# Kernel tuning notes

Measured on AMD Instinct MI355X. Metric: run time of the kernel, lower is better.

Reference implementation:

```python
import jax, jax.numpy as jnp
from jax import lax
import numpy as np

# Model hyperparameters (match init_kwargs)
DIM = 128
D_STATE = 16
D_CONV = 4
EXPAND = 2
NSLICES = 4
D_INNER = DIM * EXPAND        # 256
DT_RANK = DIM // 16           # 8
B_SZ, H_IMG, W_IMG = 2, 64, 64


def setup_inputs() -> dict:
    key = jax.random.key(0)
    ks = jax.random.split(key, 32)
    def nrm(i, shape, s=0.02):
        return jax.random.normal(ks[i], shape, jnp.float32) * s
    A_init = jnp.log(jnp.tile(jnp.arange(1, D_STATE + 1, dtype=jnp.float32)[None, :], (D_INNER, 1)))
    inp = {}
    inp["x"] = jax.random.normal(ks[0], (B_SZ, DIM, H_IMG, W_IMG), jnp.float32)
    inp["ln_w"] = jnp.ones((DIM,), jnp.float32)
    inp["ln_b"] = jnp.zeros((DIM,), jnp.float32)
    inp["in_proj_w"] = nrm(1, (2 * D_INNER, DIM))
    i = 2
    for s in ("f", "b", "s"):
        inp[f"conv_w_{s}"] = nrm(i, (D_INNER, 1, D_CONV), 0.1); i += 1
        inp[f"conv_b_{s}"] = jnp.zeros((D_INNER,), jnp.float32)
        inp[f"xproj_w_{s}"] = nrm(i, (DT_RANK + 2 * D_STATE, D_INNER)); i += 1
        inp[f"dtproj_w_{s}"] = nrm(i, (D_INNER, DT_RANK), 0.1); i += 1
        inp[f"dtproj_b_{s}"] = nrm(i, (D_INNER,), 0.1) - 4.0; i += 1  # softplus -> small dt
        inp[f"A_log_{s}"] = A_init
        inp[f"D_{s}"] = jnp.ones((D_INNER,), jnp.float32)
    inp["out_proj_w"] = nrm(i, (DIM, D_INNER)); i += 1
    inp["fuse1_w"] = nrm(i, (DIM, 2 * DIM, 3, 3), 0.05); i += 1
    inp["fuse1_b"] = jnp.zeros((DIM,), jnp.float32)
    inp["fuse2_w"] = nrm(i, (DIM, 2 * DIM, 3, 3), 0.05); i += 1
    inp["fuse2_b"] = jnp.zeros((DIM,), jnp.float32)
    return inp


def causal_conv1d(u, w, b):
    # u: (B, L, d); depthwise causal conv over L, kernel (d, 1, K)
    xc = jnp.swapaxes(u, 1, 2)  # (B, d, L)
    xc = jnp.pad(xc, ((0, 0), (0, 0), (w.shape[-1] - 1, 0)))
    y = lax.conv_general_dilated(xc, w, (1,), 'VALID',
                                 dimension_numbers=('NCH', 'OIH', 'NCH'),
                                 feature_group_count=w.shape[0])
    return jnp.swapaxes(y, 1, 2) + b


def selective_scan(u, delta, A, Bm, Cm, D):
    # u, delta: (B, L, d); A: (d, n); Bm, Cm: (B, L, n)
    dA = jnp.exp(delta[..., None] * A)                       # (B, L, d, n)
    dBu = (delta * u)[..., None] * Bm[:, :, None, :]         # (B, L, d, n)
    dA = jnp.moveaxis(dA, 1, 0)                              # (L, B, d, n)
    dBu = jnp.moveaxis(dBu, 1, 0)
    def step(h, xs):
        a, bu = xs
        h = a * h + bu
        return h, h
    h0 = jnp.zeros(dA.shape[1:], dA.dtype)
    _, hs = lax.scan(step, h0, (dA, dBu))                    # hs: (L, B, d, n)
    y = jnp.einsum('lbdn,bln->bld', hs, Cm)
    return y + u * D


def mamba_branch(u, cw, cb, xw, dw, db, A_log, D):
    # u: (B, L, d_inner)
    uc = jax.nn.silu(causal_conv1d(u, cw, cb))
    proj = uc @ xw.T                                         # (B, L, dt_rank + 2*n)
    dt = proj[..., :DT_RANK]
    Bm = proj[..., DT_RANK:DT_RANK + D_STATE]
    Cm = proj[..., DT_RANK + D_STATE:]
    delta = jax.nn.softplus(dt @ dw.T + db)
    return selective_scan(uc, delta, -jnp.exp(A_log), Bm, Cm, D)


def conv2d_3x3(x, w, b):
    y = lax.conv_general_dilated(x, w, (1, 1), ((1, 1), (1, 1)),
                                 dimension_numbers=('NCHW', 'OIHW', 'NCHW'))
    return y + b[None, :, None, None]


def reference(x, ln_w, ln_b, in_proj_w,
              conv_w_f, conv_b_f, xproj_w_f, dtproj_w_f, dtproj_b_f, A_log_f, D_f,
              conv_w_b, conv_b_b, xproj_w_b, dtproj_w_b, dtproj_b_b, A_log_b, D_b,
              conv_w_s, conv_b_s, xproj_w_s, dtproj_w_s, dtproj_b_s, A_log_s, D_s,
              out_proj_w, fuse1_w, fuse1_b, fuse2_w, fuse2_b):
    Bn, C, H, W = x.shape
    L = H * W
    xf = jnp.swapaxes(x.reshape(Bn, C, L), 1, 2)             # (B, L, C)
    mu = xf.mean(-1, keepdims=True)
    var = xf.var(-1, keepdims=True)
    xn = (xf - mu) / jnp.sqrt(var + 1e-5) * ln_w + ln_b
    xz = xn @ in_proj_w.T                                    # (B, L, 2*d_inner)
    u, z = xz[..., :D_INNER], xz[..., D_INNER:]
    # bimamba v3: forward, backward, and slice-permuted scans
    perm = jnp.arange(L).reshape(NSLICES, L // NSLICES).T.reshape(-1)
    inv = jnp.argsort(perm)
    y_f = mamba_branch(u, conv_w_f, conv_b_f, xproj_w_f, dtproj_w_f, dtproj_b_f, A_log_f, D_f)
    y_b = mamba_branch(u[:, ::-1], conv_w_b, conv_b_b, xproj_w_b, dtproj_w_b, dtproj_b_b, A_log_b, D_b)[:, ::-1]
    y_s = mamba_branch(u[:, perm], conv_w_s, conv_b_s, xproj_w_s, dtproj_w_s, dtproj_b_s, A_log_s, D_s)[:, inv]
    q, k, v = y_f, y_b, y_s                                  # (B, L, d_inner) each
    y = (y_f + y_b + y_s) * jax.nn.silu(z)
    out = y @ out_proj_w.T                                   # (B, L, dim)
    # channel-wise global attention: (q^T k) softmax over channels, then v @ attn^T
    attn = jax.nn.softmax(jnp.einsum('bld,ble->bde', q, k), axis=-1)  # (B, D, D)
    out_a = jnp.einsum('bld,bed->ble', v, attn)              # (B, L, d_inner)
    out_a = out_a.reshape(Bn, -1, H, W)                      # matches torch .view(B,-1,H,W)
    out_a = conv2d_3x3(out_a, fuse1_w, fuse1_b)              # (B, dim, H, W)
    out_m = jnp.swapaxes(out, 1, 2).reshape(Bn, C, H, W)
    o = conv2d_3x3(jnp.concatenate([out_a, out_m], axis=1), fuse2_w, fuse2_b)
    return o + x
```

## Files before the change

### kernel.cpp

```cpp
#include <hip/hip_runtime.h>
#include <math.h>

#define B_SZ 2
#define CDIM 128
#define LSEQ 4096
#define DIN  256
#define NPROJ 40
#define NCH  128
#define CHL  (LSEQ / NCH)
#define KSPL 16
#define DIRPJ 327680

typedef float f32x4 __attribute__((ext_vector_type(4)));
typedef short s16x8 __attribute__((ext_vector_type(8)));

__device__ __forceinline__ float silu_f(float v) { return v / (1.f + __expf(-v)); }

__device__ __forceinline__ unsigned short f2bf(float x) {
  unsigned int u = __float_as_uint(x);
  u += 0x7fff + ((u >> 16) & 1);
  return (unsigned short)(u >> 16);
}
__device__ __forceinline__ float bf2f(unsigned short u) {
  return __uint_as_float(((unsigned int)u) << 16);
// ... 52 lines not shown
    #pragma unroll 8
    for (int j = 0; j < 32; ++j) { float v = sx[part * 32 + j][row]; s += v; s2 += v * v; }
    s += __shfl_xor(s, 1); s += __shfl_xor(s, 2);
    s2 += __shfl_xor(s2, 1); s2 += __shfl_xor(s2, 2);
    float mu = s * (1.f / 128.f);
    float rstd = rsqrtf(s2 * (1.f / 128.f) - mu * mu + 1e-5f);
    unsigned short* o = xnbf + ((size_t)bb * 4096 + t0 + row) * 128 + part * 32;
    #pragma unroll
    for (int j = 0; j < 32; j += 2) {
      int c = part * 32 + j;
      float v0 = (sx[c][row] - mu) * rstd * lnw[c] + lnb[c];
      float v1 = (sx[c + 1][row] - mu) * rstd * lnw[c + 1] + lnb[c + 1];
      unsigned int pk = (unsigned int)f2bf(v0) | ((unsigned int)f2bf(v1) << 16);
      *(unsigned int*)(o + j) = pk;
    }
  } else {
    int zi = (bx - 960) * 256 + tid;
    ((uint4*)padz)[zi] = make_uint4(0, 0, 0, 0);
  }
}

__global__ __launch_bounds__(256) void gemm_mfma_nt(
    const unsigned short* __restrict__ A, const unsigned short* __restrict__ Bm,
    float* __restrict__ C, unsigned short* __restrict__ Cbf, int M, int N, int K,
    long sAb, long sBb, long sCb, int mode, int chofs) {
  A += (long)blockIdx.z * sAb; Bm += (long)blockIdx.z * sBb;
  if (mode == 1) Cbf += (long)blockIdx.z * sCb;
  else if (mode == 0) C += (long)blockIdx.z * sCb;
  int m0 = blockIdx.x * 64, n0 = blockIdx.y * 64;
  int tid = threadIdx.x;
  int wv = tid >> 6, lane = tid & 63, col = lane & 15, g = lane >> 4;
  __shared__ unsigned short As[8192];
  __shared__ unsigned short Bs[8192];
  f32x4 acc[4] = {};
  for (int k0 = 0; k0 < K; k0 += 128) {
    __syncthreads();
    #pragma unroll
    for (int i = 0; i < 4; ++i) {
      int s = tid + i * 256;
      int m = s >> 4, kg = s & 15;
      int off = (m * 256 + kg * 16) ^ ((m & 7) << 4);
      uint4 va = *(const uint4*)(A + (size_t)(m0 + m) * K + k0 + kg * 8);
      *(uint4*)((char*)As + off) = va;
      uint4 vb = *(const uint4*)(Bm + (size_t)(n0 + m) * K + k0 + kg * 8);
      *(uint4*)((char*)Bs + off) = vb;
    }
    __syncthreads();
    #pragma unroll
    for (int ks = 0; ks < 4; ++ks) {
      int arow = wv * 16 + col;
      s16x8 a = *(const s16x8*)((const char*)As +
                 ((arow * 256 + ks * 64 + g * 16) ^ ((col & 7) << 4)));
      #pragma unroll
      for (int nf = 0; nf < 4; ++nf) {
        int brow = nf * 16 + col;
        s16x8 bf = *(const s16x8*)((const char*)Bs +
                   ((brow * 256 + ks * 64 + g * 16) ^ ((col & 7) << 4)));
        acc[nf] = __builtin_amdgcn_mfma_f32_16x16x32_bf16(a, bf, acc[nf], 0, 0, 0);
      }
    }
  }
  #pragma unroll
  for (int nf = 0; nf < 4; ++nf) {
    #pragma unroll
    for (int r = 0; r < 4; ++r) {
      int m = m0 + wv * 16 + g * 4 + r;
      int n = n0 + nf * 16 + col;
      if (n >= N) continue;
      if (mode == 0) C[(size_t)m * N + n] = acc[nf][r];
      else if (mode == 1) Cbf[(size_t)m * N + n] = f2bf(acc[nf][r]);
      else {
        int b2 = blockIdx.z + (m >> 12);
        int sp = m & 4095;
        size_t o = (((size_t)b2 * 66 + (sp >> 6) + 1) * 66 + (sp & 63) + 1) * 256 + chofs + n;
        Cbf[o] = f2bf(acc[nf][r]);
      }
    }
  }
}

__global__ __launch_bounds__(256) void gemm_xc(
    const unsigned short* __restrict__ xzbf,
    const float* __restrict__ cw0, const float* __restrict__ cw1, const float* __restrict__ cw2,
    const float* __restrict__ cb0, const float* __restrict__ cb1, const float* __restrict__ cb2,
    const unsigned short* __restrict__ xwpackbf,
    float* __restrict__ proj, unsigned short* __restrict__ ucbf) {
  int dir = blockIdx.z;
  int m0 = blockIdx.x * 64;
  int tid = threadIdx.x;
  int wv = tid >> 6, lane = tid & 63, col = lane & 15, g = lane >> 4;
  const float* cw = dir == 0 ? cw0 : dir == 1 ? cw1 : cw2;
  const float* cb = dir == 0 ? cb0 : dir == 1 ? cb1 : cb2;
  __shared__ unsigned short As[8192];
  __shared__ unsigned short Bs[8192];
  __shared__ float scw[256 * 5];
  #pragma unroll
  for (int t = 0; t < 4; ++t) scw[tid * 5 + t] = cw[tid * 4 + t];
  scw[tid * 5 + 4] = cb[tid];
  const unsigned short* xwd = xwpackbf + dir * 16384;
// ... 40 lines not shown
      int arow = wv * 16 + col;
      s16x8 a = *(const s16x8*)((const char*)As +
                 ((arow * 256 + ks * 64 + g * 16) ^ ((col & 7) << 4)));
      #pragma unroll
      for (int nf = 0; nf < 4; ++nf) {
        int brow = nf * 16 + col;
        s16x8 bf = *(const s16x8*)((const char*)Bs +
                   ((brow * 256 + ks * 64 + g * 16) ^ ((col & 7) << 4)));
        acc[nf] = __builtin_amdgcn_mfma_f32_16x16x32_bf16(a, bf, acc[nf], 0, 0, 0);
      }
    }
  }
  #pragma unroll
  for (int nf = 0; nf < 4; ++nf) {
    #pragma unroll
    for (int r = 0; r < 4; ++r) {
      int m = m0 + wv * 16 + g * 4 + r;
      int n = nf * 16 + col;
      if (n < NPROJ) proj[(size_t)dir * DIRPJ + (size_t)m * NPROJ + n] = acc[nf][r];
    }
  }
}

__global__ __launch_bounds__(256) void post_scan(
    const unsigned short* __restrict__ ybf, const unsigned short* __restrict__ xzbf,
    const unsigned short* __restrict__ Bm, unsigned short* __restrict__ Cbf,
    unsigned short* __restrict__ yT) {
  __shared__ unsigned short As[8192];
  __shared__ unsigned short Bs[8192];
  __shared__ unsigned short T[64][72];
  int id = blockIdx.x;
  int tid = threadIdx.x;
  if (id >= 256) {
    int t = id - 256;
    int lt = t & 63, rest = t >> 6;
    int dt = rest & 3, p = rest >> 2;
    int l0 = lt * 64, d0 = dt * 64;
    const unsigned short* src = ybf + ((size_t)p * 4096) * 256;
    #pragma unroll
    for (int i = 0; i < 2; ++i) {
      int idx = tid + i * 256;
      int l = idx >> 3, dg = idx & 7;
      uint4 v = *(const uint4*)(src + (size_t)(l0 + l) * 256 + d0 + dg * 8);
      const unsigned short* pv = (const unsigned short*)&v;
      #pragma unroll
      for (int j = 0; j < 8; ++j) T[dg * 8 + j][l] = pv[j];
    }
    __syncthreads();
    #pragma unroll
    for (int i = 0; i < 2; ++i) {
      int idx = tid + i * 256;
      int d = idx >> 3, lg = idx & 7;
      uint4 v = *(const uint4*)&T[d][lg * 8];
      *(uint4*)(yT + ((size_t)p * 256 + d0 + d) * 4096 + l0 + lg * 8) = v;
    }
    return;
  }
  const size_t ds = (size_t)B_SZ * LSEQ * DIN;
  int m0 = (id >> 1) * 64, n0 = (id & 1) * 64;
  int wv = tid >> 6, lane = tid & 63, col = lane & 15, g = lane >> 4;
  f32x4 acc[4] = {};
  for (int k0 = 0; k0 < 256; k0 += 128) {
    __syncthreads();
    #pragma unroll
    for (int i = 0; i < 4; ++i) {
      int s = tid + i * 256;
      int m = s >> 4, kg = s & 15;
      size_t row = m0 + m;
      size_t ai = row * 256 + k0 + kg * 8;
      uint4 va = *(const uint4*)(ybf + ai);
      uint4 vb = *(const uint4*)(ybf + ds + ai);
      uint4 vc = *(const uint4*)(ybf + 2 * ds + ai);
      uint4 vz = *(const uint4*)(xzbf + row * 512 + 256 + k0 + kg * 8);
      const unsigned short* pa = (const unsigned short*)&va;
      const unsigned short* pb = (const unsigned short*)&vb;
      const unsigned short* pc = (const unsigned short*)&vc;
      const unsigned short* pz = (const unsigned short*)&vz;
      unsigned int pk[4];
      #pragma unroll
      for (int j = 0; j < 8; j += 2) {
        float w0 = (bf2f(pa[j]) + bf2f(pb[j]) + bf2f(pc[j])) * silu_f(bf2f(pz[j]));
        float w1 = (bf2f(pa[j+1]) + bf2f(pb[j+1]) + bf2f(pc[j+1])) * silu_f(bf2f(pz[j+1]));
        pk[j >> 1] = (unsigned int)f2bf(w0) | ((unsigned int)f2bf(w1) << 16);
      }
      int off = (m * 256 + kg * 16) ^ ((m & 7) << 4);
      *(uint4*)((char*)As + off) = make_uint4(pk[0], pk[1], pk[2], pk[3]);
      uint4 wb = *(const uint4*)(Bm + (size_t)(n0 + m) * 256 + k0 + kg * 8);
      *(uint4*)((char*)Bs + off) = wb;
    }
    __syncthreads();
    #pragma unroll
    for (int ks = 0; ks < 4; ++ks) {
      int arow = wv * 16 + col;
      s16x8 a = *(const s16x8*)((const char*)As +
                 ((arow * 256 + ks * 64 + g * 16) ^ ((col & 7) << 4)));
      #pragma unroll
      for (int nf = 0; nf < 4; ++nf) {
        int brow = nf * 16 + col;
        s16x8 bf = *(const s16x8*)((const char*)Bs +
                   ((brow * 256 + ks * 64 + g * 16) ^ ((col & 7) << 4)));
        acc[nf] = __builtin_amdgcn_mfma_f32_16x16x32_bf16(a, bf, acc[nf], 0, 0, 0);
      }
    }
  }
  #pragma unroll
  for (int nf = 0; nf < 4; ++nf) {
    #pragma unroll
    for (int r = 0; r < 4; ++r) {
      int m = m0 + wv * 16 + g * 4 + r;
      int n = n0 + nf * 16 + col;
      int b2 = m >> 12;
      int sp = m & 4095;
      size_t o = (((size_t)b2 * 66 + (sp >> 6) + 1) * 66 + (sp & 63) + 1) * 256 + 128 + n;
      Cbf[o] = f2bf(acc[nf][r]);
    }
  }
}

__global__ __launch_bounds__(256) void gemm_ts(
    const unsigned short* __restrict__ yT, float* __restrict__ P) {
  int bz = blockIdx.z;
  int b = bz / KSPL, s = bz % KSPL;
  const unsigned short* A  = yT + (size_t)b * 256 * 4096;
  const unsigned short* Bm = yT + (size_t)(2 + b) * 256 * 4096;
  float* Pb = P + (size_t)bz * 65536;
  int m0 = blockIdx.x * 64, n0 = blockIdx.y * 64;
  int tid = threadIdx.x;
  int wv = tid >> 6, lane = tid & 63, col = lane & 15, g = lane >> 4;
  __shared__ unsigned short As[8192];
  __shared__ unsigned short Bs[8192];
  f32x4 acc[4] = {};
  int kb = s * 256;
  for (int k0 = kb; k0 < kb + 256; k0 += 128) {
    __syncthreads();
    #pragma unroll
    for (int i = 0; i < 4; ++i) {
      int sI = tid + i * 256;
      int m = sI >> 4, kg = sI & 15;
      int off = (m * 256 + kg * 16) ^ ((m & 7) << 4);
      uint4 va = *(const uint4*)(A + (size_t)(m0 + m) * 4096 + k0 + kg * 8);
      *(uint4*)((char*)As + off) = va;
      uint4 vb = *(const uint4*)(Bm + (size_t)(n0 + m) * 4096 + k0 + kg * 8);
      *(uint4*)((char*)Bs + off) = vb;
    }
    __syncthreads();
    #pragma unroll
    for (int ks = 0; ks < 4; ++ks) {
      int arow = wv * 16 + col;
      s16x8 a = *(const s16x8*)((const char*)As +
                 ((arow * 256 + ks * 64 + g * 16) ^ ((col & 7) << 4)));
      #pragma unroll
      for (int nf = 0; nf < 4; ++nf) {
        int brow = nf * 16 + col;
        s16x8 bf = *(const s16x8*)((const char*)Bs +
                   ((brow * 256 + ks * 64 + g * 16) ^ ((col & 7) << 4)));
        acc[nf] = __builtin_amdgcn_mfma_f32_16x16x32_bf16(a, bf, acc[nf], 0, 0, 0);
      }
    }
  }
  #pragma unroll
  for (int nf = 0; nf < 4; ++nf)
    #pragma unroll
    for (int r = 0; r < 4; ++r) {
      int m = m0 + wv * 16 + g * 4 + r;
      int n = n0 + nf * 16 + col;
      Pb[(size_t)m * 256 + n] = acc[nf][r];
    }
}

__global__ __launch_bounds__(256) void attn_reduce_softmax(
    const float* __restrict__ P, unsigned short* __restrict__ attnbf) {
  int row = blockIdx.x;
  int b = row >> 8, d = row & 255;
  int t = threadIdx.x;
  const float* p = P + ((size_t)b * KSPL) * 65536 + (size_t)d * 256 + t;
  float v = 0.f;
  #pragma unroll
  for (int s = 0; s < KSPL; ++s) v += p[(size_t)s * 65536];
  __shared__ float red[256];
  red[t] = v; __syncthreads();
  for (int s = 128; s > 0; s >>= 1) { if (t < s) red[t] = fmaxf(red[t], red[t + s]); __syncthreads(); }
  float mx = red[0]; __syncthreads();
  float e = __expf(v - mx);
  red[t] = e; __syncthreads();
  for (int s = 128; s > 0; s >>= 1) { if (t < s) red[t] += red[t + s]; __syncthreads(); }
  attnbf[(size_t)row * 256 + t] = f2bf(e / red[0]);
}

__global__ __launch_bounds__(256) void scan_part1(
    const unsigned short* __restrict__ uc, const float* __restrict__ proj,
    const float* __restrict__ al0, const float* __restrict__ al1, const float* __restrict__ al2,
    const float* __restrict__ dw0, const float* __restrict__ dw1, const float* __restrict__ dw2,
    const float* __restrict__ db0, const float* __restrict__ db1, const float* __restrict__ db2,
    float* __restrict__ hend, float* __restrict__ sdsum) {
  int chunk = blockIdx.x, b = blockIdx.y, dir = blockIdx.z;
  int d = threadIdx.x;
  const float* alog = dir == 0 ? al0 : dir == 1 ? al1 : al2;
  const float* dwp  = dir == 0 ? dw0 : dir == 1 ? dw1 : dw2;
  const float* dbp  = dir == 0 ? db0 : dir == 1 ? db1 : db2;
  float An0 = -__expf(alog[d * 16]) * 1.44269504f;
  float dwr[8];
  #pragma unroll
  for (int i = 0; i < 8; ++i) dwr[i] = dwp[d * 8 + i];
  float dbv = dbp[d];
  size_t base = (((size_t)dir * B_SZ + b) * LSEQ + (size_t)chunk * CHL);
  const unsigned short* ucp = uc + base * DIN + d;
  const float* prj = proj + base * NPROJ;
  __shared__ float sPr[CHL][NPROJ];
  for (int i = threadIdx.x; i < CHL * NPROJ; i += 256)
    sPr[i / NPROJ][i % NPROJ] = prj[i];
  __syncthreads();
  float h[16];
  #pragma unroll
  for (int n = 0; n < 16; ++n) h[n] = 0.f;
  float sd = 0.f;
  float uv = bf2f(ucp[0]);
  for (int l = 0; l < CHL; ++l) {
    float uvn = (l + 1 < CHL) ? bf2f(ucp[(size_t)(l + 1) * DIN]) : 0.f;
    float a = dbv;
    #pragma unroll
    for (int i = 0; i < 8; ++i) a += sPr[l][i] * dwr[i];
    float dv = a > 20.f ? a : __logf(1.f + __expf(a));
    sd += dv;
    float du = dv * uv;
    float p = exp2f(dv * An0);
    float p2 = p * p, p4 = p2 * p2;
    float dA0 = p, dA1 = p2, dA2 = p2 * p, dA3 = p4;
    const float4* bp = (const float4*)&sPr[l][8];
    #pragma unroll
    for (int q = 0; q < 4; ++q) {
      float4 bb = bp[q];
      h[q*4+0] = dA0 * h[q*4+0] + du * bb.x;
      h[q*4+1] = dA1 * h[q*4+1] + du * bb.y;
      h[q*4+2] = dA2 * h[q*4+2] + du * bb.z;
      h[q*4+3] = dA3 * h[q*4+3] + du * bb.w;
      if (q < 3) { dA0 *= p4; dA1 *= p4; dA2 *= p4; dA3 *= p4; }
    }
    uv = uvn;
  }
  size_t so = (((size_t)(dir * B_SZ + b) * NCH + chunk) * DIN + d);
  float4* hp = (float4*)(hend + so * 16);
  #pragma unroll
  for (int q = 0; q < 4; ++q) hp[q] = make_float4(h[q*4+0], h[q*4+1], h[q*4+2], h[q*4+3]);
  sdsum[so] = sd;
}

__global__ __launch_bounds__(256) void scan_combine(
    const float* __restrict__ sdsum,
    const float* __restrict__ al0, const float* __restrict__ al1, const float* __restrict__ al2,
    float* __restrict__ hend) {
  int b = blockIdx.y, dir = blockIdx.z;
  int t = threadIdx.x, g = t >> 4, n = t & 15;
  int d = blockIdx.x * 16 + g;
  const float* alog = dir == 0 ? al0 : dir == 1 ? al1 : al2;
  float A2 = -__expf(alog[d * 16 + n]) * 1.44269504f;
  float h = 0.f;
  for (int c = 0; c < NCH; ++c) {
    size_t so = (((size_t)(dir * B_SZ + b) * NCH + c) * DIN + d);
    float old = hend[so * 16 + n];
    float prod = exp2f(sdsum[so] * A2);
    hend[so * 16 + n] = h;
    h = prod * h + old;
  }
}

__global__ __launch_bounds__(256) void scan_part3(
    const unsigned short* __restrict__ uc, const float* __restrict__ proj,
    const float* __restrict__ hin,
    const float* __restrict__ al0, const float* __restrict__ al1, const float* __restrict__ al2,
    const float* __restrict__ dw0, const float* __restrict__ dw1, const float* __restrict__ dw2,
    const float* __restrict__ db0, const float* __restrict__ db1, const float* __restrict__ db2,
    const float* __restrict__ D0, const float* __restrict__ D1, const float* __restrict__ D2,
    unsigned short* __restrict__ ybf) {
  int chunk = blockIdx.x, b = blockIdx.y, dir = blockIdx.z;
  int d = threadIdx.x;
  const float* alog = dir == 0 ? al0 : dir == 1 ? al1 : al2;
  const float* dwp  = dir == 0 ? dw0 : dir == 1 ? dw1 : dw2;
  const float* dbp  = dir == 0 ? db0 : dir == 1 ? db1 : db2;
  const float* Dp   = dir == 0 ? D0 : dir == 1 ? D1 : D2;
  float An0 = -__expf(alog[d * 16]) * 1.44269504f;
  float dwr[8];
  #pragma unroll
  for (int i = 0; i < 8; ++i) dwr[i] = dwp[d * 8 + i];
  float dbv = dbp[d];
  float Dd = Dp[d];
  size_t base0 = ((size_t)dir * B_SZ + b) * LSEQ;
  size_t base = base0 + (size_t)chunk * CHL;
  const unsigned short* ucp = uc + base * DIN + d;
  const float* prj = proj + base * NPROJ;
  unsigned short* yp = ybf + base0 * DIN;
  __shared__ float sPr[CHL][NPROJ];
  for (int i = threadIdx.x; i < CHL * NPROJ; i += 256)
    sPr[i / NPROJ][i % NPROJ] = prj[i];
  __syncthreads();
  size_t so = (((size_t)(dir * B_SZ + b) * NCH + chunk) * DIN + d);
  float h[16];
  const float4* hp = (const float4*)(hin + so * 16);
  #pragma unroll
  for (int q = 0; q < 4; ++q) { float4 v = hp[q]; h[q*4+0]=v.x; h[q*4+1]=v.y; h[q*4+2]=v.z; h[q*4+3]=v.w; }
  float uv = bf2f(ucp[0]);
  for (int l = 0; l < CHL; ++l) {
    float uvn = (l + 1 < CHL) ? bf2f(ucp[(size_t)(l + 1) * DIN]) : 0.f;
    float a = dbv;
    #pragma unroll
    for (int i = 0; i < 8; ++i) a += sPr[l][i] * dwr[i];
    float dv = a > 20.f ? a : __logf(1.f + __expf(a));
    float du = dv * uv;
    float p = exp2f(dv * An0);
    float p2 = p * p, p4 = p2 * p2;
    float dA0 = p, dA1 = p2, dA2 = p2 * p, dA3 = p4;
    const float4* bp = (const float4*)&sPr[l][8];
    const float4* cp = (const float4*)&sPr[l][24];
    float acc0 = 0.f, acc1 = 0.f, acc2 = 0.f, acc3 = 0.f;
    #pragma unroll
    for (int q = 0; q < 4; ++q) {
      float4 bb = bp[q]; float4 cc = cp[q];
      float h0 = dA0 * h[q*4+0] + du * bb.x;
      float h1 = dA1 * h[q*4+1] + du * bb.y;
      float h2 = dA2 * h[q*4+2] + du * bb.z;
      float h3 = dA3 * h[q*4+3] + du * bb.w;
      acc0 += h0 * cc.x; acc1 += h1 * cc.y; acc2 += h2 * cc.z; acc3 += h3 * cc.w;
      h[q*4+0] = h0; h[q*4+1] = h1; h[q*4+2] = h2; h[q*4+3] = h3;
      if (q < 3) { dA0 *= p4; dA1 *= p4; dA2 *= p4; dA3 *= p4; }
    }
    float yv = (acc0 + acc1) + (acc2 + acc3) + uv * Dd;
    int gl = chunk * CHL + l;
    int fl = dir == 0 ? gl : dir == 1 ? (LSEQ - 1 - gl) : ((gl & 3) * 1024 + (gl >> 2));
    yp[(size_t)fl * DIN + d] = f2bf(yv);
    uv = uvn;
  }
}

__global__ __launch_bounds__(256) void conv_mfma(
    const unsigned short* __restrict__ inpad, const unsigned short* __restrict__ Wb,
    const float* __restrict__ bias, const float* __restrict__ resid,
    float* __restrict__ outf, unsigned short* __restrict__ outbf, int mode) {
  int h = blockIdx.x;
  int cohalf = blockIdx.y >> 1, whalf = blockIdx.y & 1;
  int b = blockIdx.z;
  int tid = threadIdx.x;
  int wv = tid >> 6, lane = tid & 63;
  int col = lane & 15, g = lane >> 4;
  int co0 = cohalf * 64 + wv * 16;
  int w0 = whalf * 32;
  __shared__ unsigned short lds[3 * 34 * 64];
  f32x4 acc[2] = {};
  for (int cb = 0; cb < 4; ++cb) {
    __syncthreads();
    for (int s = tid; s < 816; s += 256) {
      int row = s / 272; int rem = s % 272; int c = rem >> 3; int cig = rem & 7;
      const unsigned short* gp = inpad +
          ((((size_t)b * 66 + h + row) * 66 + (w0 + c)) * 256 + cb * 64 + cig * 8);
// ... 36 lines not shown
  } else {
    #pragma unroll
    for (int t = 0; t < 2; ++t) {
      int w = w0 + t * 16 + col;
      float v0 = acc[t][0] + bias[co0 + g * 4];
      float v1 = acc[t][1] + bias[co0 + g * 4 + 1];
      float v2 = acc[t][2] + bias[co0 + g * 4 + 2];
      float v3 = acc[t][3] + bias[co0 + g * 4 + 3];
      unsigned int q0 = (unsigned int)f2bf(v0) | ((unsigned int)f2bf(v1) << 16);
      unsigned int q1 = (unsigned int)f2bf(v2) | ((unsigned int)f2bf(v3) << 16);
      size_t o = (((size_t)b * 66 + h + 1) * 66 + (w + 1)) * 256 + co0 + g * 4;
      *(uint2*)(outbf + o) = make_uint2(q0, q1);
    }
  }
}

extern "C" void kernel_launch(void* const* d_in, const int* in_sizes, int n_in,
                              void* d_out, int out_size, void* d_ws, size_t ws_size,
                              hipStream_t stream) {
  const float* x        = (const float*)d_in[0];
  const float* ln_w     = (const float*)d_in[1];
  const float* ln_b     = (const float*)d_in[2];
  const float* in_proj  = (const float*)d_in[3];
  const float* cw[3]  = {(const float*)d_in[4],  (const float*)d_in[11], (const float*)d_in[18]};
  const float* cb[3]  = {(const float*)d_in[5],  (const float*)d_in[12], (const float*)d_in[19]};
  const float* xw[3]  = {(const float*)d_in[6],  (const float*)d_in[13], (const float*)d_in[20]};
  const float* dw[3]  = {(const float*)d_in[7],  (const float*)d_in[14], (const float*)d_in[21]};
  const float* db[3]  = {(const float*)d_in[8],  (const float*)d_in[15], (const float*)d_in[22]};
  const float* al[3]  = {(const float*)d_in[9],  (const float*)d_in[16], (const float*)d_in[23]};
  const float* Dp[3]  = {(const float*)d_in[10], (const float*)d_in[17], (const float*)d_in[24]};
  const float* out_proj = (const float*)d_in[25];
  const float* f1w = (const float*)d_in[26];
  const float* f1b = (const float*)d_in[27];
  const float* f2w = (const float*)d_in[28];
  const float* f2b = (const float*)d_in[29];
  float* out = (float*)d_out;

  float* ws = (float*)d_ws;
  unsigned short* xnbf = (unsigned short*)ws;
  unsigned short* wipb = (unsigned short*)(ws + 524288);
  unsigned short* wopb = (unsigned short*)(ws + 557056);
  unsigned short* Wb1  = (unsigned short*)(ws + 573440);
  unsigned short* Wb2  = (unsigned short*)(ws + 720896);
  unsigned short* xwpackbf = (unsigned short*)(ws + 868352);
  unsigned short* xzbf = (unsigned short*)(ws + 1048576);
  unsigned short* ucbf = (unsigned short*)(ws + 3145728);
  float* proj  = ws + 6291456;
  float* hend  = ws + 7274496;
  float* sdsum = ws + 10420224;
  unsigned short* ybf = (unsigned short*)(ws + 10616832);
  float* attP  = ws + 13762560;
  unsigned short* attnbf = (unsigned short*)(ws + 15859712);
  unsigned short* inpad1 = (unsigned short*)(ws + 15925248);
  unsigned short* inpad2 = (unsigned short*)(ws + 17040384);
  unsigned short* yT = (unsigned short*)(ws + 18155520);

  const long dirUC = (long)B_SZ * LSEQ * DIN;

  mega_prep<<<dim3(3138), 256, 0, stream>>>(in_proj, out_proj, f1w, f2w,
      xw[0], xw[1], xw[2], x, ln_w, ln_b,
      wipb, wopb, Wb1, Wb2, xwpackbf, xnbf, inpad1);
  gemm_mfma_nt<<<dim3(128, 8, 1), 256, 0, stream>>>(xnbf, wipb, nullptr, xzbf,
      8192, 512, 128, 0, 0, 0, 1, 0);
  gemm_xc<<<dim3(128, 1, 3), 256, 0, stream>>>(xzbf,
      cw[0], cw[1], cw[2], cb[0], cb[1], cb[2], xwpackbf, proj, ucbf);
  scan_part1<<<dim3(NCH, B_SZ, 3), 256, 0, stream>>>(ucbf, proj,
      al[0], al[1], al[2], dw[0], dw[1], dw[2], db[0], db[1], db[2], hend, sdsum);
  scan_combine<<<dim3(16, B_SZ, 3), 256, 0, stream>>>(sdsum, al[0], al[1], al[2], hend);
  scan_part3<<<dim3(NCH, B_SZ, 3), 256, 0, stream>>>(ucbf, proj, hend,
      al[0], al[1], al[2], dw[0], dw[1], dw[2], db[0], db[1], db[2],
      Dp[0], Dp[1], Dp[2], ybf);
  post_scan<<<dim3(1280), 256, 0, stream>>>(ybf, xzbf, wopb, inpad2, yT);
  gemm_ts<<<dim3(4, 4, B_SZ * KSPL), 256, 0, stream>>>(yT, attP);
  attn_reduce_softmax<<<dim3(B_SZ * 256), 256, 0, stream>>>(attP, attnbf);
  gemm_mfma_nt<<<dim3(64, 4, B_SZ), 256, 0, stream>>>(ybf + 2 * dirUC, attnbf, nullptr, inpad1,
      4096, 256, 256, (long)LSEQ * DIN, 65536, 0, 2, 0);
  conv_mfma<<<dim3(64, 4, B_SZ), 256, 0, stream>>>(inpad1, Wb1, f1b, nullptr, nullptr, inpad2, 1);
  conv_mfma<<<dim3(64, 4, B_SZ), 256, 0, stream>>>(inpad2, Wb2, f2b, x, out, nullptr, 0);
}
```

Baseline: 291.3 us.

## Fuse scan stages and post-scan stages into cooperative kernels with grid syncs

Merges the three chunked-scan kernels (part1, combine, part3) into one cooperative kernel that uses grid-wide syncs and keeps u in shared memory between passes. It also merges out-proj, the channel-attention GEMM (now reading ybf directly with an in-LDS transpose instead of a separate yT buffer), the softmax and the attention-apply GEMM into one cooperative kernel. The aim is to cut launch overhead and intermediate traffic. In exchange it needs every block to be co-resident, adds larger shared memory (32 KB su) that may lower occupancy, and does scattered 2-byte LDS stores for the transpose.

```diff
diff --git a/kernel.cpp b/kernel.cpp
--- a/kernel.cpp
+++ b/kernel.cpp
@@ -1,5 +1,8 @@
 #include <hip/hip_runtime.h>
+#include <hip/hip_cooperative_groups.h>
 #include <math.h>
+
+namespace cg = cooperative_groups;
 
 #define B_SZ 2
 #define CDIM 128
@@ -98,11 +101,7 @@
 
 __global__ __launch_bounds__(256) void gemm_mfma_nt(
     const unsigned short* __restrict__ A, const unsigned short* __restrict__ Bm,
-    float* __restrict__ C, unsigned short* __restrict__ Cbf, int M, int N, int K,
-    long sAb, long sBb, long sCb, int mode, int chofs) {
-  A += (long)blockIdx.z * sAb; Bm += (long)blockIdx.z * sBb;
-  if (mode == 1) Cbf += (long)blockIdx.z * sCb;
-  else if (mode == 0) C += (long)blockIdx.z * sCb;
+    unsigned short* __restrict__ Cbf, int M, int N, int K) {
   int m0 = blockIdx.x * 64, n0 = blockIdx.y * 64;
   int tid = threadIdx.x;
   int wv = tid >> 6, lane = tid & 63, col = lane & 15, g = lane >> 4;
@@ -142,15 +141,7 @@
     for (int r = 0; r < 4; ++r) {
       int m = m0 + wv * 16 + g * 4 + r;
       int n = n0 + nf * 16 + col;
-      if (n >= N) continue;
-      if (mode == 0) C[(size_t)m * N + n] = acc[nf][r];
-      else if (mode == 1) Cbf[(size_t)m * N + n] = f2bf(acc[nf][r]);
-      else {
-        int b2 = blockIdx.z + (m >> 12);
-        int sp = m & 4095;
-        size_t o = (((size_t)b2 * 66 + (sp >> 6) + 1) * 66 + (sp & 63) + 1) * 256 + chofs + n;
-        Cbf[o] = f2bf(acc[nf][r]);
-      }
+      if (n < N) Cbf[(size_t)m * N + n] = f2bf(acc[nf][r]);
     }
   }
 }
@@ -237,256 +228,14 @@
   }
 }
 
-__global__ __launch_bounds__(256) void post_scan(
-    const unsigned short* __restrict__ ybf, const unsigned short* __restrict__ xzbf,
-    const unsigned short* __restrict__ Bm, unsigned short* __restrict__ Cbf,
-    unsigned short* __restrict__ yT) {
-  __shared__ unsigned short As[8192];
-  __shared__ unsigned short Bs[8192];
-  __shared__ unsigned short T[64][72];
-  int id = blockIdx.x;
-  int tid = threadIdx.x;
-  if (id >= 256) {
-    int t = id - 256;
-    int lt = t & 63, rest = t >> 6;
-    int dt = rest & 3, p = rest >> 2;
-    int l0 = lt * 64, d0 = dt * 64;
-    const unsigned short* src = ybf + ((size_t)p * 4096) * 256;
-    #pragma unroll
-    for (int i = 0; i < 2; ++i) {
-      int idx = tid + i * 256;
-      int l = idx >> 3, dg = idx & 7;
-      uint4 v = *(const uint4*)(src + (size_t)(l0 + l) * 256 + d0 + dg * 8);
-      const unsigned short* pv = (const unsigned short*)&v;
-      #pragma unroll
-      for (int j = 0; j < 8; ++j) T[dg * 8 + j][l] = pv[j];
-    }
-    __syncthreads();
-    #pragma unroll
-    for (int i = 0; i < 2; ++i) {
-      int idx = tid + i * 256;
-      int d = idx >> 3, lg = idx & 7;
-      uint4 v = *(const uint4*)&T[d][lg * 8];
-      *(uint4*)(yT + ((size_t)p * 256 + d0 + d) * 4096 + l0 + lg * 8) = v;
-    }
-    return;
-  }
-  const size_t ds = (size_t)B_SZ * LSEQ * DIN;
-  int m0 = (id >> 1) * 64, n0 = (id & 1) * 64;
-  int wv = tid >> 6, lane = tid & 63, col = lane & 15, g = lane >> 4;
-  f32x4 acc[4] = {};
-  for (int k0 = 0; k0 < 256; k0 += 128) {
-    __syncthreads();
-    #pragma unroll
-    for (int i = 0; i < 4; ++i) {
-      int s = tid + i * 256;
-      int m = s >> 4, kg = s & 15;
-      size_t row = m0 + m;
-      size_t ai = row * 256 + k0 + kg * 8;
-      uint4 va = *(const uint4*)(ybf + ai);
-      uint4 vb = *(const uint4*)(ybf + ds + ai);
-      uint4 vc = *(const uint4*)(ybf + 2 * ds + ai);
-      uint4 vz = *(const uint4*)(xzbf + row * 512 + 256 + k0 + kg * 8);
-      const unsigned short* pa = (const unsigned short*)&va;
-      const unsigned short* pb = (const unsigned short*)&vb;
-      const unsigned short* pc = (const unsigned short*)&vc;
-      const unsigned short* pz = (const unsigned short*)&vz;
-      unsigned int pk[4];
-      #pragma unroll
-      for (int j = 0; j < 8; j += 2) {
-        float w0 = (bf2f(pa[j]) + bf2f(pb[j]) + bf2f(pc[j])) * silu_f(bf2f(pz[j]));
-        float w1 = (bf2f(pa[j+1]) + bf2f(pb[j+1]) + bf2f(pc[j+1])) * silu_f(bf2f(pz[j+1]));
-        pk[j >> 1] = (unsigned int)f2bf(w0) | ((unsigned int)f2bf(w1) << 16);
-      }
-      int off = (m * 256 + kg * 16) ^ ((m & 7) << 4);
-      *(uint4*)((char*)As + off) = make_uint4(pk[0], pk[1], pk[2], pk[3]);
-      uint4 wb = *(const uint4*)(Bm + (size_t)(n0 + m) * 256 + k0 + kg * 8);
-      *(uint4*)((char*)Bs + off) = wb;
-    }
-    __syncthreads();
-    #pragma unroll
-    for (int ks = 0; ks < 4; ++ks) {
-      int arow = wv * 16 + col;
-      s16x8 a = *(const s16x8*)((const char*)As +
-                 ((arow * 256 + ks * 64 + g * 16) ^ ((col & 7) << 4)));
-      #pragma unroll
-      for (int nf = 0; nf < 4; ++nf) {
-        int brow = nf * 16 + col;
-        s16x8 bf = *(const s16x8*)((const char*)Bs +
-                   ((brow * 256 + ks * 64 + g * 16) ^ ((col & 7) << 4)));
-        acc[nf] = __builtin_amdgcn_mfma_f32_16x16x32_bf16(a, bf, acc[nf], 0, 0, 0);
-      }
-    }
-  }
-  #pragma unroll
-  for (int nf = 0; nf < 4; ++nf) {
-    #pragma unroll
-    for (int r = 0; r < 4; ++r) {
-      int m = m0 + wv * 16 + g * 4 + r;
-      int n = n0 + nf * 16 + col;
-      int b2 = m >> 12;
-      int sp = m & 4095;
-      size_t o = (((size_t)b2 * 66 + (sp >> 6) + 1) * 66 + (sp & 63) + 1) * 256 + 128 + n;
-      Cbf[o] = f2bf(acc[nf][r]);
-    }
-  }
-}
-
-__global__ __launch_bounds__(256) void gemm_ts(
-    const unsigned short* __restrict__ yT, float* __restrict__ P) {
-  int bz = blockIdx.z;
-  int b = bz / KSPL, s = bz % KSPL;
-  const unsigned short* A  = yT + (size_t)b * 256 * 4096;
-  const unsigned short* Bm = yT + (size_t)(2 + b) * 256 * 4096;
-  float* Pb = P + (size_t)bz * 65536;
-  int m0 = blockIdx.x * 64, n0 = blockIdx.y * 64;
-  int tid = threadIdx.x;
-  int wv = tid >> 6, lane = tid & 63, col = lane & 15, g = lane >> 4;
-  __shared__ unsigned short As[8192];
-  __shared__ unsigned short Bs[8192];
-  f32x4 acc[4] = {};
-  int kb = s * 256;
-  for (int k0 = kb; k0 < kb + 256; k0 += 128) {
-    __syncthreads();
-    #pragma unroll
-    for (int i = 0; i < 4; ++i) {
-      int sI = tid + i * 256;
-      int m = sI >> 4, kg = sI & 15;
-      int off = (m * 256 + kg * 16) ^ ((m & 7) << 4);
-      uint4 va = *(const uint4*)(A + (size_t)(m0 + m) * 4096 + k0 + kg * 8);
-      *(uint4*)((char*)As + off) = va;
-      uint4 vb = *(const uint4*)(Bm + (size_t)(n0 + m) * 4096 + k0 + kg * 8);
-      *(uint4*)((char*)Bs + off) = vb;
-    }
-    __syncthreads();
-    #pragma unroll
-    for (int ks = 0; ks < 4; ++ks) {
-      int arow = wv * 16 + col;
-      s16x8 a = *(const s16x8*)((const char*)As +
-                 ((arow * 256 + ks * 64 + g * 16) ^ ((col & 7) << 4)));
-      #pragma unroll
-      for (int nf = 0; nf < 4; ++nf) {
-        int brow = nf * 16 + col;
-        s16x8 bf = *(const s16x8*)((const char*)Bs +
-                   ((brow * 256 + ks * 64 + g * 16) ^ ((col & 7) << 4)));
-        acc[nf] = __builtin_amdgcn_mfma_f32_16x16x32_bf16(a, bf, acc[nf], 0, 0, 0);
-      }
-    }
-  }
-  #pragma unroll
-  for (int nf = 0; nf < 4; ++nf)
-    #pragma unroll
-    for (int r = 0; r < 4; ++r) {
-      int m = m0 + wv * 16 + g * 4 + r;
-      int n = n0 + nf * 16 + col;
-      Pb[(size_t)m * 256 + n] = acc[nf][r];
-    }
-}
-
-__global__ __launch_bounds__(256) void attn_reduce_softmax(
-    const float* __restrict__ P, unsigned short* __restrict__ attnbf) {
-  int row = blockIdx.x;
-  int b = row >> 8, d = row & 255;
-  int t = threadIdx.x;
-  const float* p = P + ((size_t)b * KSPL) * 65536 + (size_t)d * 256 + t;
-  float v = 0.f;
-  #pragma unroll
-  for (int s = 0; s < KSPL; ++s) v += p[(size_t)s * 65536];
-  __shared__ float red[256];
-  red[t] = v; __syncthreads();
-  for (int s = 128; s > 0; s >>= 1) { if (t < s) red[t] = fmaxf(red[t], red[t + s]); __syncthreads(); }
-  float mx = red[0]; __syncthreads();
-  float e = __expf(v - mx);
-  red[t] = e; __syncthreads();
-  for (int s = 128; s > 0; s >>= 1) { if (t < s) red[t] += red[t + s]; __syncthreads(); }
-  attnbf[(size_t)row * 256 + t] = f2bf(e / red[0]);
-}
-
-__global__ __launch_bounds__(256) void scan_part1(
+__global__ __launch_bounds__(256) void scan_fused(
     const unsigned short* __restrict__ uc, const float* __restrict__ proj,
     const float* __restrict__ al0, const float* __restrict__ al1, const float* __restrict__ al2,
     const float* __restrict__ dw0, const float* __restrict__ dw1, const float* __restrict__ dw2,
     const float* __restrict__ db0, const float* __restrict__ db1, const float* __restrict__ db2,
-    float* __restrict__ hend, float* __restrict__ sdsum) {
-  int chunk = blockIdx.x, b = blockIdx.y, dir = blockIdx.z;
-  int d = threadIdx.x;
-  const float* alog = dir == 0 ? al0 : dir == 1 ? al1 : al2;
-  const float* dwp  = dir == 0 ? dw0 : dir == 1 ? dw1 : dw2;
-  const float* dbp  = dir == 0 ? db0 : dir == 1 ? db1 : db2;
-  float An0 = -__expf(alog[d * 16]) * 1.44269504f;
-  float dwr[8];
-  #pragma unroll
-  for (int i = 0; i < 8; ++i) dwr[i] = dwp[d * 8 + i];
-  float dbv = dbp[d];
-  size_t base = (((size_t)dir * B_SZ + b) * LSEQ + (size_t)chunk * CHL);
-  const unsigned short* ucp = uc + base * DIN + d;
-  const float* prj = proj + base * NPROJ;
-  __shared__ float sPr[CHL][NPROJ];
-  for (int i = threadIdx.x; i < CHL * NPROJ; i += 256)
-    sPr[i / NPROJ][i % NPROJ] = prj[i];
-  __syncthreads();
-  float h[16];
-  #pragma unroll
-  for (int n = 0; n < 16; ++n) h[n] = 0.f;
-  float sd = 0.f;
-  float uv = bf2f(ucp[0]);
-  for (int l = 0; l < CHL; ++l) {
-    float uvn = (l + 1 < CHL) ? bf2f(ucp[(size_t)(l + 1) * DIN]) : 0.f;
-    float a = dbv;
-    #pragma unroll
-    for (int i = 0; i < 8; ++i) a += sPr[l][i] * dwr[i];
-    float dv = a > 20.f ? a : __logf(1.f + __expf(a));
-    sd += dv;
-    float du = dv * uv;
-    float p = exp2f(dv * An0);
-    float p2 = p * p, p4 = p2 * p2;
-    float dA0 = p, dA1 = p2, dA2 = p2 * p, dA3 = p4;
-    const float4* bp = (const float4*)&sPr[l][8];
-    #pragma unroll
-    for (int q = 0; q < 4; ++q) {
-      float4 bb = bp[q];
-      h[q*4+0] = dA0 * h[q*4+0] + du * bb.x;
-      h[q*4+1] = dA1 * h[q*4+1] + du * bb.y;
-      h[q*4+2] = dA2 * h[q*4+2] + du * bb.z;
-      h[q*4+3] = dA3 * h[q*4+3] + du * bb.w;
-      if (q < 3) { dA0 *= p4; dA1 *= p4; dA2 *= p4; dA3 *= p4; }
-    }
-    uv = uvn;
-  }
-  size_t so = (((size_t)(dir * B_SZ + b) * NCH + chunk) * DIN + d);
-  float4* hp = (float4*)(hend + so * 16);
-  #pragma unroll
-  for (int q = 0; q < 4; ++q) hp[q] = make_float4(h[q*4+0], h[q*4+1], h[q*4+2], h[q*4+3]);
-  sdsum[so] = sd;
-}
-
-__global__ __launch_bounds__(256) void scan_combine(
-    const float* __restrict__ sdsum,
-    const float* __restrict__ al0, const float* __restrict__ al1, const float* __restrict__ al2,
-    float* __restrict__ hend) {
-  int b = blockIdx.y, dir = blockIdx.z;
-  int t = threadIdx.x, g = t >> 4, n = t & 15;
-  int d = blockIdx.x * 16 + g;
-  const float* alog = dir == 0 ? al0 : dir == 1 ? al1 : al2;
-  float A2 = -__expf(alog[d * 16 + n]) * 1.44269504f;
-  float h = 0.f;
-  for (int c = 0; c < NCH; ++c) {
-    size_t so = (((size_t)(dir * B_SZ + b) * NCH + c) * DIN + d);
-    float old = hend[so * 16 + n];
-    float prod = exp2f(sdsum[so] * A2);
-    hend[so * 16 + n] = h;
-    h = prod * h + old;
-  }
-}
-
-__global__ __launch_bounds__(256) void scan_part3(
-    const unsigned short* __restrict__ uc, const float* __restrict__ proj,
-    const float* __restrict__ hin,
-    const float* __restrict__ al0, const float* __restrict__ al1, const float* __restrict__ al2,
-    const float* __restrict__ dw0, const float* __restrict__ dw1, const float* __restrict__ dw2,
-    const float* __restrict__ db0, const float* __restrict__ db1, const float* __restrict__ db2,
     const float* __restrict__ D0, const float* __restrict__ D1, const float* __restrict__ D2,
-    unsigned short* __restrict__ ybf) {
+    float* __restrict__ hend, float* __restrict__ sdsum, unsigned short* __restrict__ ybf) {
+  cg::grid_group gg = cg::this_grid();
   int chunk = blockIdx.x, b = blockIdx.y, dir = blockIdx.z;
   int d = threadIdx.x;
   const float* alog = dir == 0 ? al0 : dir == 1 ? al1 : al2;
@@ -503,19 +252,68 @@
   size_t base = base0 + (size_t)chunk * CHL;
   const unsigned short* ucp = uc + base * DIN + d;
   const float* prj = proj + base * NPROJ;
-  unsigned short* yp = ybf + base0 * DIN;
   __shared__ float sPr[CHL][NPROJ];
+  __shared__ float su[CHL][256];
   for (int i = threadIdx.x; i < CHL * NPROJ; i += 256)
     sPr[i / NPROJ][i % NPROJ] = prj[i];
   __syncthreads();
+  float h[16];
+  #pragma unroll
+  for (int n = 0; n < 16; ++n) h[n] = 0.f;
+  float sd = 0.f;
+  for (int l = 0; l < CHL; ++l) {
+    float uv = bf2f(ucp[(size_t)l * DIN]);
+    su[l][d] = uv;
+    float a = dbv;
+    #pragma unroll
+    for (int i = 0; i < 8; ++i) a += sPr[l][i] * dwr[i];
+    float dv = a > 20.f ? a : __logf(1.f + __expf(a));
+    sd += dv;
+    float du = dv * uv;
+    float p = exp2f(dv * An0);
+    float p2 = p * p, p4 = p2 * p2;
+    float dA0 = p, dA1 = p2, dA2 = p2 * p, dA3 = p4;
+    const float4* bp = (const float4*)&sPr[l][8];
+    #pragma unroll
+    for (int q = 0; q < 4; ++q) {
+      float4 bb = bp[q];
+      h[q*4+0] = dA0 * h[q*4+0] + du * bb.x;
+      h[q*4+1] = dA1 * h[q*4+1] + du * bb.y;
+      h[q*4+2] = dA2 * h[q*4+2] + du * bb.z;
+      h[q*4+3] = dA3 * h[q*4+3] + du * bb.w;
+      if (q < 3) { dA0 *= p4; dA1 *= p4; dA2 *= p4; dA3 *= p4; }
+    }
+  }
   size_t so = (((size_t)(dir * B_SZ + b) * NCH + chunk) * DIN + d);
-  float h[16];
-  const float4* hp = (const float4*)(hin + so * 16);
-  #pragma unroll
-  for (int q = 0; q < 4; ++q) { float4 v = hp[q]; h[q*4+0]=v.x; h[q*4+1]=v.y; h[q*4+2]=v.z; h[q*4+3]=v.w; }
-  float uv = bf2f(ucp[0]);
+  {
+    float4* hp = (float4*)(hend + so * 16);
+    #pragma unroll
+    for (int q = 0; q < 4; ++q) hp[q] = make_float4(h[q*4+0], h[q*4+1], h[q*4+2], h[q*4+3]);
+    sdsum[so] = sd;
+  }
+  gg.sync();
+  if (chunk < 16) {
+    int g = d >> 4, n = d & 15;
+    int dd = chunk * 16 + g;
+    float A2 = -__expf(alog[dd * 16 + n]) * 1.44269504f;
+    float hh = 0.f;
+    for (int c = 0; c < NCH; ++c) {
+      size_t so2 = (((size_t)(dir * B_SZ + b) * NCH + c) * DIN + dd);
+      float old = hend[so2 * 16 + n];
+      float prod = exp2f(sdsum[so2] * A2);
+      hend[so2 * 16 + n] = hh;
+      hh = prod * hh + old;
+    }
+  }
+  gg.sync();
+  {
+    const float4* hp = (const float4*)(hend + so * 16);
+    #pragma unroll
+    for (int q = 0; q < 4; ++q) { float4 v = hp[q]; h[q*4+0]=v.x; h[q*4+1]=v.y; h[q*4+2]=v.z; h[q*4+3]=v.w; }
+  }
+  unsigned short* yp = ybf + base0 * DIN;
   for (int l = 0; l < CHL; ++l) {
-    float uvn = (l + 1 < CHL) ? bf2f(ucp[(size_t)(l + 1) * DIN]) : 0.f;
+    float uv = su[l][d];
     float a = dbv;
     #pragma unroll
     for (int i = 0; i < 8; ++i) a += sPr[l][i] * dwr[i];
@@ -542,7 +340,191 @@
     int gl = chunk * CHL + l;
     int fl = dir == 0 ? gl : dir == 1 ? (LSEQ - 1 - gl) : ((gl & 3) * 1024 + (gl >> 2));
     yp[(size_t)fl * DIN + d] = f2bf(yv);
-    uv = uvn;
+  }
+}
+
+__global__ __launch_bounds__(256) void post_mega(
+    const unsigned short* __restrict__ ybf, const unsigned short* __restrict__ xzbf,
+    const unsigned short* __restrict__ wopb, unsigned short* __restrict__ inpad2,
+    float* __restrict__ attP, unsigned short* __restrict__ attnbf,
+    unsigned short* __restrict__ inpad1) {
+  cg::grid_group gg = cg::this_grid();
+  __shared__ unsigned short As[8192];
+  __shared__ unsigned short Bs[8192];
+  __shared__ float red[256];
+  int id = blockIdx.x, tid = threadIdx.x;
+  int wv = tid >> 6, lane = tid & 63, col = lane & 15, g = lane >> 4;
+  const size_t ds = (size_t)B_SZ * LSEQ * DIN;
+  if (id < 256) {
+    int m0 = (id >> 1) * 64, n0 = (id & 1) * 64;
+    f32x4 acc[4] = {};
+    for (int k0 = 0; k0 < 256; k0 += 128) {
+      __syncthreads();
+      #pragma unroll
+      for (int i = 0; i < 4; ++i) {
+        int s = tid + i * 256;
+        int m = s >> 4, kg = s & 15;
+        size_t row = m0 + m;
+        size_t ai = row * 256 + k0 + kg * 8;
+        uint4 va = *(const uint4*)(ybf + ai);
+        uint4 vb = *(const uint4*)(ybf + ds + ai);
+        uint4 vc = *(const uint4*)(ybf + 2 * ds + ai);
+        uint4 vz = *(const uint4*)(xzbf + row * 512 + 256 + k0 + kg * 8);
+        const unsigned short* pa = (const unsigned short*)&va;
+        const unsigned short* pb = (const unsigned short*)&vb;
+        const unsigned short* pc = (const unsigned short*)&vc;
+        const unsigned short* pz = (const unsigned short*)&vz;
+        unsigned int pk[4];
+        #pragma unroll
+        for (int j = 0; j < 8; j += 2) {
+          float w0 = (bf2f(pa[j]) + bf2f(pb[j]) + bf2f(pc[j])) * silu_f(bf2f(pz[j]));
+          float w1 = (bf2f(pa[j+1]) + bf2f(pb[j+1]) + bf2f(pc[j+1])) * silu_f(bf2f(pz[j+1]));
+          pk[j >> 1] = (unsigned int)f2bf(w0) | ((unsigned int)f2bf(w1) << 16);
+        }
+        int off = (m * 256 + kg * 16) ^ ((m & 7) << 4);
+        *(uint4*)((char*)As + off) = make_uint4(pk[0], pk[1], pk[2], pk[3]);
+        uint4 wb = *(const uint4*)(wopb + (size_t)(n0 + m) * 256 + k0 + kg * 8);
+        *(uint4*)((char*)Bs + off) = wb;
+      }
+      __syncthreads();
+      #pragma unroll
+      for (int ks = 0; ks < 4; ++ks) {
+        int arow = wv * 16 + col;
+        s16x8 a = *(const s16x8*)((const char*)As +
+                   ((arow * 256 + ks * 64 + g * 16) ^ ((col & 7) << 4)));
+        #pragma unroll
+        for (int nf = 0; nf < 4; ++nf) {
+          int brow = nf * 16 + col;
+          s16x8 bf = *(const s16x8*)((const char*)Bs +
+                     ((brow * 256 + ks * 64 + g * 16) ^ ((col & 7) << 4)));
+          acc[nf] = __builtin_amdgcn_mfma_f32_16x16x32_bf16(a, bf, acc[nf], 0, 0, 0);
+        }
+      }
+    }
+    #pragma unroll
+    for (int nf = 0; nf < 4; ++nf) {
+      #pragma unroll
+      for (int r = 0; r < 4; ++r) {
+        int m = m0 + wv * 16 + g * 4 + r;
+        int n = n0 + nf * 16 + col;
+        int b2 = m >> 12;
+        int sp = m & 4095;
+        size_t o = (((size_t)b2 * 66 + (sp >> 6) + 1) * 66 + (sp & 63) + 1) * 256 + 128 + n;
+        inpad2[o] = f2bf(acc[nf][r]);
+      }
+    }
+  } else {
+    int t2 = id - 256;
+    int mx = t2 & 3, nx = (t2 >> 2) & 3, bz = t2 >> 4;
+    int bq = bz / KSPL, sq = bz % KSPL;
+    const unsigned short* Ap = ybf + ((size_t)bq * LSEQ) * DIN;
+    const unsigned short* Bp = ybf + ((size_t)(B_SZ + bq) * LSEQ) * DIN;
+    float* Pb = attP + (size_t)bz * 65536;
+    int m0 = mx * 64, n0 = nx * 64;
+    f32x4 acc[4] = {};
+    int kb = sq * 256;
+    for (int k0 = kb; k0 < kb + 256; k0 += 128) {
+      __syncthreads();
+      #pragma unroll
+      for (int i = 0; i < 4; ++i) {
+        int sI = tid + i * 256;
+        int l = sI >> 3, dg = sI & 7;
+        uint4 va = *(const uint4*)(Ap + (size_t)(k0 + l) * 256 + m0 + dg * 8);
+        uint4 vb = *(const uint4*)(Bp + (size_t)(k0 + l) * 256 + n0 + dg * 8);
+        const unsigned short* pa = (const unsigned short*)&va;
+        const unsigned short* pb = (const unsigned short*)&vb;
+        #pragma unroll
+        for (int j = 0; j < 8; ++j) {
+          int row = dg * 8 + j;
+          int off = (row * 256 + l * 2) ^ ((row & 7) << 4);
+          *(unsigned short*)((char*)As + off) = pa[j];
+          *(unsigned short*)((char*)Bs + off) = pb[j];
+        }
+      }
+      __syncthreads();
+      #pragma unroll
+      for (int ks = 0; ks < 4; ++ks) {
+        int arow = wv * 16 + col;
+        s16x8 a = *(const s16x8*)((const char*)As +
+                   ((arow * 256 + ks * 64 + g * 16) ^ ((col & 7) << 4)));
+        #pragma unroll
+        for (int nf = 0; nf < 4; ++nf) {
+          int brow = nf * 16 + col;
+          s16x8 bf = *(const s16x8*)((const char*)Bs +
+                     ((brow * 256 + ks * 64 + g * 16) ^ ((col & 7) << 4)));
+          acc[nf] = __builtin_amdgcn_mfma_f32_16x16x32_bf16(a, bf, acc[nf], 0, 0, 0);
+        }
+      }
+    }
+    #pragma unroll
+    for (int nf = 0; nf < 4; ++nf)
+      #pragma unroll
+      for (int r = 0; r < 4; ++r) {
+        int m = m0 + wv * 16 + g * 4 + r;
+        int n = n0 + nf * 16 + col;
+        Pb[(size_t)m * 256 + n] = acc[nf][r];
+      }
+  }
+  gg.sync();
+  if (id < 512) {
+    int b = id >> 8, dd = id & 255;
+    const float* p = attP + ((size_t)b * KSPL) * 65536 + (size_t)dd * 256 + tid;
+    float v = 0.f;
+    #pragma unroll
+    for (int s = 0; s < KSPL; ++s) v += p[(size_t)s * 65536];
+    red[tid] = v; __syncthreads();
+    for (int s = 128; s > 0; s >>= 1) { if (tid < s) red[tid] = fmaxf(red[tid], red[tid + s]); __syncthreads(); }
+    float mx = red[0]; __syncthreads();
+    float e = __expf(v - mx);
+    red[tid] = e; __syncthreads();
+    for (int s = 128; s > 0; s >>= 1) { if (tid < s) red[tid] += red[tid + s]; __syncthreads(); }
+    attnbf[(size_t)id * 256 + tid] = f2bf(e / red[0]);
+  }
+  gg.sync();
+  if (id < 512) {
+    int bx = id & 63, by = (id >> 6) & 3, bz = id >> 8;
+    const unsigned short* A = ybf + 2 * ds + (size_t)bz * LSEQ * DIN;
+    const unsigned short* Bm = attnbf + (size_t)bz * 65536;
+    int m0 = bx * 64, n0 = by * 64;
+    f32x4 acc[4] = {};
+    for (int k0 = 0; k0 < 256; k0 += 128) {
+      __syncthreads();
+      #pragma unroll
+      for (int i = 0; i < 4; ++i) {
+        int s = tid + i * 256;
+        int m = s >> 4, kg = s & 15;
+        int off = (m * 256 + kg * 16) ^ ((m & 7) << 4);
+        uint4 va = *(const uint4*)(A + (size_t)(m0 + m) * 256 + k0 + kg * 8);
+        *(uint4*)((char*)As + off) = va;
+        uint4 vb = *(const uint4*)(Bm + (size_t)(n0 + m) * 256 + k0 + kg * 8);
+        *(uint4*)((char*)Bs + off) = vb;
+      }
+      __syncthreads();
+      #pragma unroll
+      for (int ks = 0; ks < 4; ++ks) {
+        int arow = wv * 16 + col;
+        s16x8 a = *(const s16x8*)((const char*)As +
+                   ((arow * 256 + ks * 64 + g * 16) ^ ((col & 7) << 4)));
+        #pragma unroll
+        for (int nf = 0; nf < 4; ++nf) {
+          int brow = nf * 16 + col;
+          s16x8 bf = *(const s16x8*)((const char*)Bs +
+                     ((brow * 256 + ks * 64 + g * 16) ^ ((col & 7) << 4)));
+          acc[nf] = __builtin_amdgcn_mfma_f32_16x16x32_bf16(a, bf, acc[nf], 0, 0, 0);
+        }
+      }
+    }
+    #pragma unroll
+    for (int nf = 0; nf < 4; ++nf) {
+      #pragma unroll
+      for (int r = 0; r < 4; ++r) {
+        int m = m0 + wv * 16 + g * 4 + r;
+        int n = n0 + nf * 16 + col;
+        int sp = m & 4095;
+        size_t o = (((size_t)bz * 66 + (sp >> 6) + 1) * 66 + (sp & 63) + 1) * 256 + n;
+        inpad1[o] = f2bf(acc[nf][r]);
+      }
+    }
   }
 }
 
@@ -625,13 +607,13 @@
   const float* ln_w     = (const float*)d_in[1];
   const float* ln_b     = (const float*)d_in[2];
   const float* in_proj  = (const float*)d_in[3];
-  const float* cw[3]  = {(const float*)d_in[4],  (const float*)d_in[11], (const float*)d_in[18]};
-  const float* cb[3]  = {(const float*)d_in[5],  (const float*)d_in[12], (const float*)d_in[19]};
-  const float* xw[3]  = {(const float*)d_in[6],  (const float*)d_in[13], (const float*)d_in[20]};
-  const float* dw[3]  = {(const float*)d_in[7],  (const float*)d_in[14], (const float*)d_in[21]};
-  const float* db[3]  = {(const float*)d_in[8],  (const float*)d_in[15], (const float*)d_in[22]};
-  const float* al[3]  = {(const float*)d_in[9],  (const float*)d_in[16], (const float*)d_in[23]};
-  const float* Dp[3]  = {(const float*)d_in[10], (const float*)d_in[17], (const float*)d_in[24]};
+  const float* cw0 = (const float*)d_in[4],  *cw1 = (const float*)d_in[11], *cw2 = (const float*)d_in[18];
+  const float* cb0 = (const float*)d_in[5],  *cb1 = (const float*)d_in[12], *cb2 = (const float*)d_in[19];
+  const float* xw0 = (const float*)d_in[6],  *xw1 = (const float*)d_in[13], *xw2 = (const float*)d_in[20];
+  const float* dw0 = (const float*)d_in[7],  *dw1 = (const float*)d_in[14], *dw2 = (const float*)d_in[21];
+  const float* db0 = (const float*)d_in[8],  *db1 = (const float*)d_in[15], *db2 = (const float*)d_in[22];
+  const float* al0 = (const float*)d_in[9],  *al1 = (const float*)d_in[16], *al2 = (const float*)d_in[23];
+  const float* Dp0 = (const float*)d_in[10], *Dp1 = (const float*)d_in[17], *Dp2 = (const float*)d_in[24];
   const float* out_proj = (const float*)d_in[25];
   const float* f1w = (const float*)d_in[26];
   const float* f1b = (const float*)d_in[27];
@@ -656,28 +638,27 @@
   unsigned short* attnbf = (unsigned short*)(ws + 15859712);
   unsigned short* inpad1 = (unsigned short*)(ws + 15925248);
   unsigned short* inpad2 = (unsigned short*)(ws + 17040384);
-  unsigned short* yT = (unsigned short*)(ws + 18155520);
-
-  const long dirUC = (long)B_SZ * LSEQ * DIN;
 
   mega_prep<<<dim3(3138), 256, 0, stream>>>(in_proj, out_proj, f1w, f2w,
-      xw[0], xw[1], xw[2], x, ln_w, ln_b,
+      xw0, xw1, xw2, x, ln_w, ln_b,
       wipb, wopb, Wb1, Wb2, xwpackbf, xnbf, inpad1);
-  gemm_mfma_nt<<<dim3(128, 8, 1), 256, 0, stream>>>(xnbf, wipb, nullptr, xzbf,
-      8192, 512, 128, 0, 0, 0, 1, 0);
+  gemm_mfma_nt<<<dim3(128, 8, 1), 256, 0, stream>>>(xnbf, wipb, xzbf, 8192, 512, 128);
   gemm_xc<<<dim3(128, 1, 3), 256, 0, stream>>>(xzbf,
-      cw[0], cw[1], cw[2], cb[0], cb[1], cb[2], xwpackbf, proj, ucbf);
-  scan_part1<<<dim3(NCH, B_SZ, 3), 256, 0, stream>>>(ucbf, proj,
-      al[0], al[1], al[2], dw[0], dw[1], dw[2], db[0], db[1], db[2], hend, sdsum);
-  scan_combine<<<dim3(16, B_SZ, 3), 256, 0, stream>>>(sdsum, al[0], al[1], al[2], hend);
-  scan_part3<<<dim3(NCH, B_SZ, 3), 256, 0, stream>>>(ucbf, proj, hend,
-      al[0], al[1], al[2], dw[0], dw[1], dw[2], db[0], db[1], db[2],
-      Dp[0], Dp[1], Dp[2], ybf);
-  post_scan<<<dim3(1280), 256, 0, stream>>>(ybf, xzbf, wopb, inpad2, yT);
-  gemm_ts<<<dim3(4, 4, B_SZ * KSPL), 256, 0, stream>>>(yT, attP);
-  attn_reduce_softmax<<<dim3(B_SZ * 256), 256, 0, stream>>>(attP, attnbf);
-  gemm_mfma_nt<<<dim3(64, 4, B_SZ), 256, 0, stream>>>(ybf + 2 * dirUC, attnbf, nullptr, inpad1,
-      4096, 256, 256, (long)LSEQ * DIN, 65536, 0, 2, 0);
+      cw0, cw1, cw2, cb0, cb1, cb2, xwpackbf, proj, ucbf);
+  {
+    void* args[] = {(void*)&ucbf, (void*)&proj,
+                    (void*)&al0, (void*)&al1, (void*)&al2,
+                    (void*)&dw0, (void*)&dw1, (void*)&dw2,
+                    (void*)&db0, (void*)&db1, (void*)&db2,
+                    (void*)&Dp0, (void*)&Dp1, (void*)&Dp2,
+                    (void*)&hend, (void*)&sdsum, (void*)&ybf};
+    hipLaunchCooperativeKernel((void*)scan_fused, dim3(NCH, B_SZ, 3), dim3(256), args, 0, stream);
+  }
+  {
+    void* args[] = {(void*)&ybf, (void*)&xzbf, (void*)&wopb, (void*)&inpad2,
+                    (void*)&attP, (void*)&attnbf, (void*)&inpad1};
+    hipLaunchCooperativeKernel((void*)post_mega, dim3(768), dim3(256), args, 0, stream);
+  }
   conv_mfma<<<dim3(64, 4, B_SZ), 256, 0, stream>>>(inpad1, Wb1, f1b, nullptr, nullptr, inpad2, 1);
   conv_mfma<<<dim3(64, 4, B_SZ), 256, 0, stream>>>(inpad2, Wb2, f2b, x, out, nullptr, 0);
 }
```

New measurement: 697.7 us. 139% more time.
